# Optimization experiments

Measured on AMD Instinct MI355X. Metric: run time of the kernel, lower is better.

## Reference

```python
import jax, jax.numpy as jnp
import numpy as np

STRIDE, PAD, DIL = 1, 1, 1


def setup_inputs() -> dict:
    key = jax.random.key(0)
    ks = jax.random.split(key, 5)
    N, Cin, H, W = 8, 256, 56, 56
    Cout, kh, kw = 256, 3, 3
    x = jax.random.normal(ks[0], (N, Cin, H, W), jnp.float32)
    offset = jax.random.normal(ks[1], (N, 2 * kh * kw, H, W), jnp.float32)
    mask = jax.random.uniform(ks[2], (N, kh * kw, H, W), jnp.float32)
    fan_in = Cin * kh * kw
    bound = float(np.sqrt(6.0 / fan_in))  # kaiming_uniform, relu gain
    weight = jax.random.uniform(ks[3], (Cout, Cin, kh, kw), jnp.float32, -bound, bound)
    bias = jnp.zeros((Cout,), jnp.float32)
    return {"x": x, "offset": offset, "mask": mask, "weight": weight, "bias": bias}


def _mdcn(x, offset, mask, weight, bias):
    N, Cin, H, W = x.shape
    Cout, _, kh, kw = weight.shape
    K = kh * kw
    Hout = (H + 2 * PAD - (DIL * (kh - 1) + 1)) // STRIDE + 1
    Wout = (W + 2 * PAD - (DIL * (kw - 1) + 1)) // STRIDE + 1
    # offset channels: [K, 2(y,x)] interleaved -> [N,K,2,Hout,Wout]
    off = offset.reshape(N, K, 2, Hout, Wout)
    dy, dx = off[:, :, 0], off[:, :, 1]
    ky = (jnp.arange(K) // kw) * DIL
    kx = (jnp.arange(K) % kw) * DIL
    base_y = jnp.arange(Hout) * STRIDE - PAD
    base_x = jnp.arange(Wout) * STRIDE - PAD
    py = dy + ky[None, :, None, None] + base_y[None, None, :, None]  # [N,K,Ho,Wo]
    px = dx + kx[None, :, None, None] + base_x[None, None, None, :]
    y0 = jnp.floor(py)
    x0 = jnp.floor(px)
    wy1 = py - y0
    wx1 = px - x0
    wy0 = 1.0 - wy1
    wx0 = 1.0 - wx1
    y0i = y0.astype(jnp.int32)
    x0i = x0.astype(jnp.int32)
    x_nhwc = jnp.transpose(x, (0, 2, 3, 1))  # [N,H,W,Cin]
    nidx = jnp.arange(N)[:, None, None, None]

    def gather(yi, xi):
        valid = (yi >= 0) & (yi < H) & (xi >= 0) & (xi < W)
        yc = jnp.clip(yi, 0, H - 1)
        xc = jnp.clip(xi, 0, W - 1)
        v = x_nhwc[nidx, yc, xc]  # [N,K,Ho,Wo,Cin]
        return v * valid[..., None].astype(x.dtype)

    v = (gather(y0i, x0i) * (wy0 * wx0)[..., None]
         + gather(y0i, x0i + 1) * (wy0 * wx1)[..., None]
         + gather(y0i + 1, x0i) * (wy1 * wx0)[..., None]
         + gather(y0i + 1, x0i + 1) * (wy1 * wx1)[..., None])
    v = v * mask.reshape(N, K, Hout, Wout)[..., None]
    wr = weight.reshape(Cout, Cin, K)
    out = jnp.einsum('nkhwc,ock->nohw', v, wr)
    return out + bias[None, :, None, None]


def reference(x, offset, mask, weight, bias):
    return _mdcn(x, offset, mask, weight, bias)
```

## Files before the change

kernel.cpp:

```cpp
#include <hip/hip_runtime.h>
#include <math.h>

#define H_ 56
#define W_ 56
#define CIN 256
#define COUT 256
#define NB 8
#define SPIX 3136
#define KG 2304
#define MTOT 25088
#define MT 128
#define NBLK 196
#define GUARD_PX 2048

typedef __bf16 v8bf __attribute__((ext_vector_type(8)));
typedef float  v4f  __attribute__((ext_vector_type(4)));

#define WAIT_VM(N)  do { asm volatile("s_waitcnt vmcnt(" #N ")" ::: "memory"); \
                         __builtin_amdgcn_sched_barrier(0); } while (0)
#define WAIT_LGKM0  do { asm volatile("s_waitcnt lgkmcnt(0)" ::: "memory"); \
                         __builtin_amdgcn_sched_barrier(0); } while (0)
#define BARR        do { asm volatile("s_barrier" ::: "memory"); } while (0)

__device__ __forceinline__ void async_copy16(const void* g, void* l) {
    __builtin_amdgcn_global_load_lds(
        (const __attribute__((address_space(1))) void*)g,
        (__attribute__((address_space(3))) void*)l, 16, 0, 0);
}

__global__ __launch_bounds__(256) void prep_xw(const float* __restrict__ x,
                                               const float* __restrict__ w,
                                               __bf16* __restrict__ xb,
                                               __bf16* __restrict__ bp) {
    __shared__ float tile[64][65];
    const int tid = threadIdx.x;
    if (blockIdx.z < 8) {
        const int n = blockIdx.z, c0 = blockIdx.y * 64, s0 = blockIdx.x * 64;
        const float* xp = x + (size_t)n * CIN * SPIX;
        __bf16* xo = xb + (size_t)n * SPIX * CIN;
#pragma unroll
        for (int i = 0; i < 16; ++i) {
            int idx = tid + i * 256;
            int cr = idx >> 6, sc = idx & 63;
            tile[cr][sc] = xp[(c0 + cr) * SPIX + s0 + sc];
        }
        __syncthreads();
#pragma unroll
        for (int i = 0; i < 16; ++i) {
            int idx = tid + i * 256;
            int sr = idx >> 6, cc = idx & 63;
            xo[(s0 + sr) * CIN + c0 + cc] = (__bf16)tile[cc][sr];
        }
    } else {
        const int base = (blockIdx.y * 49 + blockIdx.x) * 256 + tid;
        for (int i = base; i < COUT * KG; i += 196 * 256) {
            const int o = i / KG;
            const int rem = i - o * KG;
            const int c = rem / 9;
            const int tap = rem - c * 9;
            bp[(size_t)o * KG + tap * 256 + c] = (__bf16)w[i];
        }
    }
}

__device__ __forceinline__ void compute_params(
    const float* __restrict__ offs, const float* __restrict__ msk,
    int m0, int* sS, float4* sW, int tid)
{
    for (int idx = tid; idx < 9 * MT; idx += 512) {
        const int tl = idx >> 7, pl = idx & 127;
        const int pg = m0 + pl;
        const int n  = pg / SPIX;
        const int s  = pg - n * SPIX;
        const int h  = s / W_, w = s - h * W_;
        const int kY = tl / 3, kX = tl - kY * 3;
        const float dy = offs[n * (18 * SPIX) + (2 * tl) * SPIX + s];
        const float dx = offs[n * (18 * SPIX) + (2 * tl + 1) * SPIX + s];
        const float mk = msk[n * (9 * SPIX) + tl * SPIX + s];
        const float py = dy + (float)(kY + h - 1);
        const float px = dx + (float)(kX + w - 1);
        const float fy0 = floorf(py), fx0 = floorf(px);
        const int y0 = (int)fy0, x0 = (int)fx0;
        const float wy1 = py - fy0, wx1 = px - fx0;
        const float wy0 = 1.f - wy1, wx0 = 1.f - wx1;
        const bool yv0 = (y0 >= 0) & (y0 < H_);
        const bool yv1 = (y0 + 1 >= 0) & (y0 + 1 < H_);
        const bool xv0 = (x0 >= 0) & (x0 < W_);
        const bool xv1 = (x0 + 1 >= 0) & (x0 + 1 < W_);
        float4 wt;
        wt.x = (yv0 & xv0) ? wy0 * wx0 * mk : 0.f;
        wt.y = (yv0 & xv1) ? wy0 * wx1 * mk : 0.f;
        wt.z = (yv1 & xv0) ? wy1 * wx0 * mk : 0.f;
        wt.w = (yv1 & xv1) ? wy1 * wx1 * mk : 0.f;
        int base = n * SPIX + y0 * W_ + x0;
        base = min(max(base, -GUARD_PX), NB * SPIX - 58 + GUARD_PX);
        sS[idx] = base * CIN;
        sW[idx] = wt;
    }
}

__global__ __launch_bounds__(512, 2) void mdcn_fused4(
    const __bf16* __restrict__ xb,
    const float*  __restrict__ offs,
    const float*  __restrict__ msk,
    const __bf16* __restrict__ bp,
    const float*  __restrict__ bias,
    float*        __restrict__ out)
{
    __shared__ __align__(16) char smem[121344];
    int*    sS = (int*)(smem + 98304);
    float4* sW = (float4*)(smem + 102912);

    const int tid  = threadIdx.x;
    const int lane = tid & 63, wv = tid >> 6;
    const int wm = wv & 1, wn = wv >> 1;
    const int l15 = lane & 15, q = lane >> 4;

    const int xcd = blockIdx.x & 7, ib = blockIdx.x >> 3;
    const int wg  = (xcd < 4) ? xcd * 25 + ib : 100 + (xcd - 4) * 24 + ib;
    const int m0  = wg * MT;

    compute_params(offs, msk, m0, sS, sW, tid);

    v4f acc[4][4];
#pragma unroll
    for (int i = 0; i < 4; ++i)
#pragma unroll
        for (int j = 0; j < 4; ++j) acc[i][j] = (v4f)0.f;

    __syncthreads();

    const int pxl = tid >> 2, c2 = tid & 3;
    v8bf ga0, ga1, ga2, ga3, gb0, gb1, gb2, gb3;
    float4 cw;

#define GATHER(E, KQ)                                                   \
    { const int b_ = sS[E] + ((KQ) << 6) + c2 * 8;                      \
      cw  = sW[E];                                                      \
      ga0 = *(const v8bf*)(xb + b_);                                    \
      ga1 = *(const v8bf*)(xb + b_ + 256);                              \
      ga2 = *(const v8bf*)(xb + b_ + 14336);                            \
      ga3 = *(const v8bf*)(xb + b_ + 14592);                            \
      gb0 = *(const v8bf*)(xb + b_ + 32);                               \
      gb1 = *(const v8bf*)(xb + b_ + 288);                              \
      gb2 = *(const v8bf*)(xb + b_ + 14368);                            \
      gb3 = *(const v8bf*)(xb + b_ + 14624); }

#define COMBINE_STORE(AP)                                               \
    { v8bf r0, r1;                                                      \
      _Pragma("unroll")                                                 \
      for (int j = 0; j < 8; ++j) {                                     \
        r0[j] = (__bf16)(cw.x * (float)ga0[j] + cw.y * (float)ga1[j]    \
                       + cw.z * (float)ga2[j] + cw.w * (float)ga3[j]);  \
        r1[j] = (__bf16)(cw.x * (float)gb0[j] + cw.y * (float)gb1[j]    \
                       + cw.z * (float)gb2[j] + cw.w * (float)gb3[j]);  \
      }                                                                 \
      *(v8bf*)((AP) + pxl * 64 + (((c2)     ^ (pxl & 7)) << 3)) = r0;   \
      *(v8bf*)((AP) + pxl * 64 + (((c2 + 4) ^ (pxl & 7)) << 3)) = r1; }

#define STAGE_B(K0, LB)                                                 \
    { _Pragma("unroll")                                                 \
      for (int t = 0; t < 4; ++t) {                                     \
        const int brow = t * 64 + (wv << 3) + (lane >> 3);              \
        const int blc  = (lane & 7) ^ (brow & 7);                       \
        async_copy16(bp + (size_t)brow * KG + (K0) + blc * 8,           \
                     (LB) + ((t * 8 + wv) << 10)); }

    GATHER(pxl, 0)
    COMBINE_STORE((__bf16*)smem)
    STAGE_B(0, smem + 32768) }
    GATHER(pxl, 1)
    WAIT_LGKM0;
    WAIT_VM(8);
    BARR;

    char* ac = smem;          char* an = smem + 16384;
    char* bc = smem + 32768;  char* bn = smem + 65536;

#pragma unroll 1
    for (int ks = 0; ks < 36; ++ks) {
        if (ks < 35) {
            STAGE_B((ks + 1) << 6, bn) }
            WAIT_VM(4);
            COMBINE_STORE((__bf16*)an)
            if (ks < 34) {
                const int st = ks + 2;
                GATHER((st >> 2) * MT + pxl, st & 3)
            }
        }

        __builtin_amdgcn_s_setprio(1);
#pragma unroll
        for (int kf = 0; kf < 2; ++kf) {
            v8bf afr[4], bfr[4];
#pragma unroll
            for (int mt = 0; mt < 4; ++mt) {
                const int row = wm * 64 + mt * 16 + l15;
                const int pch = (kf * 4 + q) ^ (row & 7);
                afr[mt] = *(const v8bf*)((__bf16*)ac + row * 64 + pch * 8);
            }
#pragma unroll
            for (int nt = 0; nt < 4; ++nt) {
                const int row = wn * 64 + nt * 16 + l15;
                const int pch = (kf * 4 + q) ^ (row & 7);
                bfr[nt] = *(const v8bf*)((__bf16*)bc + row * 64 + pch * 8);
            }
#pragma unroll
            for (int mt = 0; mt < 4; ++mt)
#pragma unroll
                for (int nt = 0; nt < 4; ++nt)
                    acc[mt][nt] = __builtin_amdgcn_mfma_f32_16x16x32_bf16(
                        afr[mt], bfr[nt], acc[mt][nt], 0, 0, 0);
        }
        __builtin_amdgcn_s_setprio(0);

        if (ks < 34) {
            WAIT_LGKM0;
            WAIT_VM(8);
            BARR;
        } else if (ks == 34) {
            WAIT_LGKM0;
            WAIT_VM(0);
            BARR;
        }
        char* t;
        t = ac; ac = an; an = t;
        t = bc; bc = bn; bn = t;
    }
#undef GATHER
#undef COMBINE_STORE
#undef STAGE_B

    WAIT_LGKM0;
    BARR;
    float* epi = (float*)smem + wv * 1104;
    const int pg_l = m0 + wm * 64 + lane;
    const int n_l  = pg_l / SPIX;
    float* outp = out + (size_t)n_l * (COUT * SPIX) + (pg_l - n_l * SPIX);

#pragma unroll
    for (int nt = 0; nt < 4; ++nt) {
        const float bv = bias[wn * 64 + nt * 16 + l15];
#pragma unroll
        for (int mt = 0; mt < 4; ++mt)
#pragma unroll
            for (int r = 0; r < 4; ++r)
                epi[(mt * 16 + q * 4 + r) * 17 + l15] = acc[mt][nt][r] + bv;
#pragma unroll
        for (int oc = 0; oc < 16; ++oc)
            outp[(size_t)(wn * 64 + nt * 16 + oc) * SPIX] = epi[lane * 17 + oc];
    }
}

#define BM 64
#define BN 64
#define BKF 32
#define AST 68
#define BST 68
#define CST 65
__global__ __launch_bounds__(256) void mdcn_fallback(
    const float* __restrict__ xs, const float* __restrict__ offs,
    const float* __restrict__ msk, const float* __restrict__ wraw,
    const float* __restrict__ bias, float* __restrict__ out)
{
    __shared__ float smem[BKF * AST + BKF * BST];
    __shared__ int   sBase[4][BM];
    __shared__ float sWgt[4][BM];
    float (*At)[AST] = (float (*)[AST])smem;
    float (*Bt)[BST] = (float (*)[BST])(smem + BKF * AST);
    float (*Cs)[CST] = (float (*)[CST])smem;
    const int tid = threadIdx.x;
    const int m0 = blockIdx.x * BM;
    const int o0 = blockIdx.y * BN;
    const int n  = m0 / SPIX;
    const int s0 = m0 - n * SPIX;
    const int tx = tid & 15, ty = tid >> 4;
    float acc[4][4] = {};
    for (int k = 0; k < 9; ++k) {
        if (tid < BM) {
            const int s = s0 + tid;
            const int h = s / W_;
            const int w = s - h * W_;
            const int kY = k / 3, kX = k - kY * 3;
            const float dy = offs[(size_t)n * (18 * SPIX) + (size_t)(2 * k) * SPIX + s];
            const float dx = offs[(size_t)n * (18 * SPIX) + (size_t)(2 * k + 1) * SPIX + s];
            const float mk = msk[(size_t)n * (9 * SPIX) + (size_t)k * SPIX + s];
            const float py = dy + (float)(kY + h - 1);
            const float px = dx + (float)(kX + w - 1);
            const float fy0 = floorf(py), fx0 = floorf(px);
            const int y0 = (int)fy0, x0 = (int)fx0;
            const float wy1 = py - fy0, wx1 = px - fx0;
            const float wy0 = 1.0f - wy1, wx0 = 1.0f - wx1;
#pragma unroll
            for (int t = 0; t < 4; ++t) {
                const int yi = y0 + (t >> 1), xi = x0 + (t & 1);
                const bool valid = (yi >= 0) & (yi < H_) & (xi >= 0) & (xi < W_);
                const int yc = min(max(yi, 0), H_ - 1);
                const int xc = min(max(xi, 0), W_ - 1);
                float wt = ((t >> 1) ? wy1 : wy0) * ((t & 1) ? wx1 : wx0) * mk;
                sBase[t][tid] = n * (CIN * SPIX) + yc * W_ + xc;
                sWgt[t][tid] = valid ? wt : 0.0f;
            }
        }
        __syncthreads();
        for (int c0 = 0; c0 < CIN; c0 += BKF) {
#pragma unroll
            for (int i = 0; i < 8; ++i) {
                int idx = tid + i * 256;
                int row = idx >> 5, cc = idx & 31;
                int ce = (c0 + cc) * SPIX;
                At[cc][row] = sWgt[0][row] * xs[sBase[0][row] + ce]
                            + sWgt[1][row] * xs[sBase[1][row] + ce]
                            + sWgt[2][row] * xs[sBase[2][row] + ce]
                            + sWgt[3][row] * xs[sBase[3][row] + ce];
            }
#pragma unroll
            for (int i = 0; i < 8; ++i) {
                int idx = tid + i * 256;
                int kf = idx >> 6, o = idx & 63;
                Bt[kf][o] = wraw[(size_t)(o0 + o) * KG + (c0 + kf) * 9 + k];
            }
            __syncthreads();
#pragma unroll
            for (int kf = 0; kf < BKF; ++kf) {
                const float4 a = *(const float4*)&At[kf][ty * 4];
                const float4 b = *(const float4*)&Bt[kf][tx * 4];
                acc[0][0] = fmaf(a.x, b.x, acc[0][0]); acc[0][1] = fmaf(a.x, b.y, acc[0][1]);
                acc[0][2] = fmaf(a.x, b.z, acc[0][2]); acc[0][3] = fmaf(a.x, b.w, acc[0][3]);
                acc[1][0] = fmaf(a.y, b.x, acc[1][0]); acc[1][1] = fmaf(a.y, b.y, acc[1][1]);
                acc[1][2] = fmaf(a.y, b.z, acc[1][2]); acc[1][3] = fmaf(a.y, b.w, acc[1][3]);
                acc[2][0] = fmaf(a.z, b.x, acc[2][0]); acc[2][1] = fmaf(a.z, b.y, acc[2][1]);
                acc[2][2] = fmaf(a.z, b.z, acc[2][2]); acc[2][3] = fmaf(a.z, b.w, acc[2][3]);
                acc[3][0] = fmaf(a.w, b.x, acc[3][0]); acc[3][1] = fmaf(a.w, b.y, acc[3][1]);
                acc[3][2] = fmaf(a.w, b.z, acc[3][2]); acc[3][3] = fmaf(a.w, b.w, acc[3][3]);
            }
            __syncthreads();
        }
    }
#pragma unroll
    for (int i = 0; i < 4; ++i)
#pragma unroll
        for (int j = 0; j < 4; ++j)
            Cs[ty * 4 + i][tx * 4 + j] = acc[i][j] + bias[o0 + tx * 4 + j];
    __syncthreads();
    const int pix = tid & 63, ob = tid >> 6;
    float* outp = out + (size_t)n * COUT * SPIX + s0 + pix;
#pragma unroll
    for (int r = 0; r < 16; ++r) {
        int o = r * 4 + ob;
        outp[(size_t)(o0 + o) * SPIX] = Cs[pix][o];
    }
}

extern "C" void kernel_launch(void* const* d_in, const int* in_sizes, int n_in,
                              void* d_out, int out_size, void* d_ws, size_t ws_size,
                              hipStream_t stream) {
    const float* x    = (const float*)d_in[0];
    const float* offs = (const float*)d_in[1];
    const float* msk  = (const float*)d_in[2];
    const float* w    = (const float*)d_in[3];
    const float* bias = (const float*)d_in[4];
    float* out = (float*)d_out;

    const size_t GUARD_B  = (size_t)GUARD_PX * CIN * sizeof(__bf16);
    const size_t xb_bytes = (size_t)NB * SPIX * CIN * sizeof(__bf16);
    const size_t bp_bytes = (size_t)KG * COUT * sizeof(__bf16);
    const size_t need     = GUARD_B + xb_bytes + GUARD_B + bp_bytes;

    if (ws_size >= need) {
        __bf16* xb = (__bf16*)((char*)d_ws + GUARD_B);
        __bf16* bp = (__bf16*)((char*)d_ws + GUARD_B + xb_bytes + GUARD_B);
        hipMemsetAsync(d_ws, 0, GUARD_B, stream);
        hipMemsetAsync((char*)d_ws + GUARD_B + xb_bytes, 0, GUARD_B, stream);
        prep_xw<<<dim3(49, 4, 9), 256, 0, stream>>>(x, w, xb, bp);
        mdcn_fused4<<<dim3(NBLK), 512, 0, stream>>>(xb, offs, msk, bp, bias, out);
    } else {
        mdcn_fallback<<<dim3(MTOT / BM, COUT / BN), 256, 0, stream>>>(
            x, offs, msk, w, bias, out);
    }
}
```

Measured before the change: 156.0 us.

## Triple-buffer weight tiles, double-register gather, fold guard memsets into prep kernel

```diff
diff --git a/kernel.cpp b/kernel.cpp
--- a/kernel.cpp
+++ b/kernel.cpp
@@ -51,7 +51,7 @@
             int sr = idx >> 6, cc = idx & 63;
             xo[(s0 + sr) * CIN + c0 + cc] = (__bf16)tile[cc][sr];
         }
-    } else {
+    } else if (blockIdx.z == 8) {
         const int base = (blockIdx.y * 49 + blockIdx.x) * 256 + tid;
         for (int i = base; i < COUT * KG; i += 196 * 256) {
             const int o = i / KG;
@@ -59,6 +59,15 @@
             const int c = rem / 9;
             const int tap = rem - c * 9;
             bp[(size_t)o * KG + tap * 256 + c] = (__bf16)w[i];
+        }
+    } else {
+        const int gtid = (blockIdx.y * 49 + blockIdx.x) * 256 + tid;
+        v8bf* lo = (v8bf*)(xb - (size_t)GUARD_PX * CIN);
+        v8bf* hi = (v8bf*)(xb + (size_t)NB * SPIX * CIN);
+        const v8bf z = (v8bf)(__bf16)0.f;
+        for (int i = gtid; i < 65536; i += 196 * 256) {
+            lo[i] = z;
+            hi[i] = z;
         }
     }
 }
@@ -99,7 +108,7 @@
     }
 }
 
-__global__ __launch_bounds__(512, 2) void mdcn_fused4(
+__global__ __launch_bounds__(512, 2) void mdcn_fused5(
     const __bf16* __restrict__ xb,
     const float*  __restrict__ offs,
     const float*  __restrict__ msk,
@@ -107,9 +116,11 @@
     const float*  __restrict__ bias,
     float*        __restrict__ out)
 {
-    __shared__ __align__(16) char smem[121344];
-    int*    sS = (int*)(smem + 98304);
-    float4* sW = (float4*)(smem + 102912);
+    __shared__ __align__(16) char smem[154112];
+    __bf16* A0 = (__bf16*)smem;
+    __bf16* A1 = (__bf16*)(smem + 16384);
+    int*    sS = (int*)(smem + 131072);
+    float4* sW = (float4*)(smem + 135680);
 
     const int tid  = threadIdx.x;
     const int lane = tid & 63, wv = tid >> 6;
@@ -130,106 +141,119 @@
 
     __syncthreads();
 
-    const int pxl = tid >> 2, c2 = tid & 3;
-    v8bf ga0, ga1, ga2, ga3, gb0, gb1, gb2, gb3;
-    float4 cw;
-
-#define GATHER(E, KQ)                                                   \
-    { const int b_ = sS[E] + ((KQ) << 6) + c2 * 8;                      \
-      cw  = sW[E];                                                      \
-      ga0 = *(const v8bf*)(xb + b_);                                    \
-      ga1 = *(const v8bf*)(xb + b_ + 256);                              \
-      ga2 = *(const v8bf*)(xb + b_ + 14336);                            \
-      ga3 = *(const v8bf*)(xb + b_ + 14592);                            \
-      gb0 = *(const v8bf*)(xb + b_ + 32);                               \
-      gb1 = *(const v8bf*)(xb + b_ + 288);                              \
-      gb2 = *(const v8bf*)(xb + b_ + 14368);                            \
-      gb3 = *(const v8bf*)(xb + b_ + 14624); }
-
-#define COMBINE_STORE(AP)                                               \
-    { v8bf r0, r1;                                                      \
-      _Pragma("unroll")                                                 \
-      for (int j = 0; j < 8; ++j) {                                     \
-        r0[j] = (__bf16)(cw.x * (float)ga0[j] + cw.y * (float)ga1[j]    \
-                       + cw.z * (float)ga2[j] + cw.w * (float)ga3[j]);  \
-        r1[j] = (__bf16)(cw.x * (float)gb0[j] + cw.y * (float)gb1[j]    \
-                       + cw.z * (float)gb2[j] + cw.w * (float)gb3[j]);  \
-      }                                                                 \
-      *(v8bf*)((AP) + pxl * 64 + (((c2)     ^ (pxl & 7)) << 3)) = r0;   \
-      *(v8bf*)((AP) + pxl * 64 + (((c2 + 4) ^ (pxl & 7)) << 3)) = r1; }
-
-#define STAGE_B(K0, LB)                                                 \
-    { _Pragma("unroll")                                                 \
-      for (int t = 0; t < 4; ++t) {                                     \
-        const int brow = t * 64 + (wv << 3) + (lane >> 3);              \
-        const int blc  = (lane & 7) ^ (brow & 7);                       \
-        async_copy16(bp + (size_t)brow * KG + (K0) + blc * 8,           \
-                     (LB) + ((t * 8 + wv) << 10)); }
-
-    GATHER(pxl, 0)
-    COMBINE_STORE((__bf16*)smem)
-    STAGE_B(0, smem + 32768) }
-    GATHER(pxl, 1)
+    const int pq = tid >> 3, c8 = tid & 7;
+    const int offA0 = pq * 64 + ((c8 ^ (pq & 7)) << 3);
+    const int offA1 = offA0 + 4096;
+    v8bf ga0A, ga1A, ga2A, ga3A, gb0A, gb1A, gb2A, gb3A;
+    v8bf ga0B, ga1B, ga2B, ga3B, gb0B, gb1B, gb2B, gb3B;
+
+#define GATHER2(S, J)                                                    \
+    { const int e0_ = ((J) >> 2) * 128 + pq;                             \
+      const int ko_ = (((J) & 3) << 6) + (c8 << 3);                      \
+      const int b0_ = sS[e0_] + ko_;                                     \
+      const int b1_ = sS[e0_ + 64] + ko_;                                \
+      ga0##S = *(const v8bf*)(xb + b0_);                                 \
+      ga1##S = *(const v8bf*)(xb + b0_ + 256);                           \
+      ga2##S = *(const v8bf*)(xb + b0_ + 14336);                         \
+      ga3##S = *(const v8bf*)(xb + b0_ + 14592);                         \
+      gb0##S = *(const v8bf*)(xb + b1_);                                 \
+      gb1##S = *(const v8bf*)(xb + b1_ + 256);                           \
+      gb2##S = *(const v8bf*)(xb + b1_ + 14336);                         \
+      gb3##S = *(const v8bf*)(xb + b1_ + 14592); }
+
+#define COMBINE2(S, J, AP)                                               \
+    { const int e0_ = ((J) >> 2) * 128 + pq;                             \
+      const float4 wa_ = sW[e0_];                                        \
+      const float4 wb_ = sW[e0_ + 64];                                   \
+      v8bf r0_, r1_;                                                     \
+      _Pragma("unroll")                                                  \
+      for (int j = 0; j < 8; ++j) {                                      \
+        r0_[j] = (__bf16)(wa_.x * (float)ga0##S[j] + wa_.y * (float)ga1##S[j] \
+                        + wa_.z * (float)ga2##S[j] + wa_.w * (float)ga3##S[j]); \
+        r1_[j] = (__bf16)(wb_.x * (float)gb0##S[j] + wb_.y * (float)gb1##S[j] \
+                        + wb_.z * (float)gb2##S[j] + wb_.w * (float)gb3##S[j]); } \
+      *(v8bf*)((AP) + offA0) = r0_;                                      \
+      *(v8bf*)((AP) + offA1) = r1_; }
+
+#define STAGE_B(K0, LB)                                                  \
+    do { _Pragma("unroll")                                               \
+      for (int t = 0; t < 4; ++t) {                                      \
+        const int brow = t * 64 + (wv << 3) + (lane >> 3);               \
+        const int blc  = (lane & 7) ^ (brow & 7);                        \
+        async_copy16(bp + (size_t)brow * KG + (K0) + blc * 8,            \
+                     (LB) + ((t * 8 + wv) << 10)); } } while (0)
+
+#define MFMA_STEP(AB, BB)                                                \
+    { __builtin_amdgcn_s_setprio(1);                                     \
+      _Pragma("unroll")                                                  \
+      for (int kf = 0; kf < 2; ++kf) {                                   \
+        v8bf afr[4], bfr[4];                                             \
+        _Pragma("unroll")                                                \
+        for (int mt = 0; mt < 4; ++mt) {                                 \
+          const int row = wm * 64 + mt * 16 + l15;                       \
+          const int pch = (kf * 4 + q) ^ (row & 7);                      \
+          afr[mt] = *(const v8bf*)((AB) + row * 64 + pch * 8); }         \
+        _Pragma("unroll")                                                \
+        for (int nt = 0; nt < 4; ++nt) {                                 \
+          const int row = wn * 64 + nt * 16 + l15;                       \
+          const int pch = (kf * 4 + q) ^ (row & 7);                      \
+          bfr[nt] = *(const v8bf*)((BB) + row * 64 + pch * 8); }         \
+        _Pragma("unroll")                                                \
+        for (int mt = 0; mt < 4; ++mt)                                   \
+          _Pragma("unroll")                                              \
+          for (int nt = 0; nt < 4; ++nt)                                 \
+            acc[mt][nt] = __builtin_amdgcn_mfma_f32_16x16x32_bf16(       \
+                afr[mt], bfr[nt], acc[mt][nt], 0, 0, 0); }               \
+      __builtin_amdgcn_s_setprio(0); }
+
+    STAGE_B(0, smem + 32768);
+    GATHER2(A, 0)
+    STAGE_B(64, smem + 65536);
+    WAIT_VM(4);
+    COMBINE2(A, 0, A0)
+    GATHER2(B, 1)
     WAIT_LGKM0;
-    WAIT_VM(8);
     BARR;
 
-    char* ac = smem;          char* an = smem + 16384;
-    char* bc = smem + 32768;  char* bn = smem + 65536;
+    __bf16* bc = (__bf16*)(smem + 32768);
+    __bf16* bn = (__bf16*)(smem + 65536);
+    __bf16* b2 = (__bf16*)(smem + 98304);
 
 #pragma unroll 1
-    for (int ks = 0; ks < 36; ++ks) {
-        if (ks < 35) {
-            STAGE_B((ks + 1) << 6, bn) }
-            WAIT_VM(4);
-            COMBINE_STORE((__bf16*)an)
-            if (ks < 34) {
-                const int st = ks + 2;
-                GATHER((st >> 2) * MT + pxl, st & 3)
-            }
-        }
-
-        __builtin_amdgcn_s_setprio(1);
-#pragma unroll
-        for (int kf = 0; kf < 2; ++kf) {
-            v8bf afr[4], bfr[4];
-#pragma unroll
-            for (int mt = 0; mt < 4; ++mt) {
-                const int row = wm * 64 + mt * 16 + l15;
-                const int pch = (kf * 4 + q) ^ (row & 7);
-                afr[mt] = *(const v8bf*)((__bf16*)ac + row * 64 + pch * 8);
-            }
-#pragma unroll
-            for (int nt = 0; nt < 4; ++nt) {
-                const int row = wn * 64 + nt * 16 + l15;
-                const int pch = (kf * 4 + q) ^ (row & 7);
-                bfr[nt] = *(const v8bf*)((__bf16*)bc + row * 64 + pch * 8);
-            }
-#pragma unroll
-            for (int mt = 0; mt < 4; ++mt)
-#pragma unroll
-                for (int nt = 0; nt < 4; ++nt)
-                    acc[mt][nt] = __builtin_amdgcn_mfma_f32_16x16x32_bf16(
-                        afr[mt], bfr[nt], acc[mt][nt], 0, 0, 0);
-        }
-        __builtin_amdgcn_s_setprio(0);
-
-        if (ks < 34) {
-            WAIT_LGKM0;
-            WAIT_VM(8);
-            BARR;
-        } else if (ks == 34) {
-            WAIT_LGKM0;
-            WAIT_VM(0);
-            BARR;
-        }
-        char* t;
-        t = ac; ac = an; an = t;
-        t = bc; bc = bn; bn = t;
-    }
-#undef GATHER
-#undef COMBINE_STORE
+    for (int k2 = 0; k2 < 17; ++k2) {
+        const int e = k2 * 2;
+        STAGE_B((size_t)(e + 2) << 6, (char*)b2);
+        GATHER2(A, e + 2)
+        WAIT_VM(12);
+        COMBINE2(B, e + 1, A1)
+        MFMA_STEP(A0, bc);
+        WAIT_LGKM0;
+        BARR;
+        { __bf16* t = bc; bc = bn; bn = b2; b2 = t; }
+
+        const int o = e + 1;
+        STAGE_B((size_t)(o + 2) << 6, (char*)b2);
+        GATHER2(B, o + 2)
+        WAIT_VM(12);
+        COMBINE2(A, o + 1, A0)
+        MFMA_STEP(A1, bc);
+        WAIT_LGKM0;
+        BARR;
+        { __bf16* t = bc; bc = bn; bn = b2; b2 = t; }
+    }
+
+    WAIT_VM(0);
+    COMBINE2(B, 35, A1)
+    MFMA_STEP(A0, bc);
+    WAIT_LGKM0;
+    BARR;
+    { __bf16* t = bc; bc = bn; bn = b2; b2 = t; }
+    MFMA_STEP(A1, bc);
+
+#undef GATHER2
+#undef COMBINE2
 #undef STAGE_B
+#undef MFMA_STEP
 
     WAIT_LGKM0;
     BARR;
@@ -370,10 +394,8 @@
     if (ws_size >= need) {
         __bf16* xb = (__bf16*)((char*)d_ws + GUARD_B);
         __bf16* bp = (__bf16*)((char*)d_ws + GUARD_B + xb_bytes + GUARD_B);
-        hipMemsetAsync(d_ws, 0, GUARD_B, stream);
-        hipMemsetAsync((char*)d_ws + GUARD_B + xb_bytes, 0, GUARD_B, stream);
-        prep_xw<<<dim3(49, 4, 9), 256, 0, stream>>>(x, w, xb, bp);
-        mdcn_fused4<<<dim3(NBLK), 512, 0, stream>>>(xb, offs, msk, bp, bias, out);
+        prep_xw<<<dim3(49, 4, 10), 256, 0, stream>>>(x, w, xb, bp);
+        mdcn_fused5<<<dim3(NBLK), 512, 0, stream>>>(xb, offs, msk, bp, bias, out);
     } else {
         mdcn_fallback<<<dim3(MTOT / BM, COUT / BN), 256, 0, stream>>>(
             x, offs, msk, w, bias, out);
```

Result: slower. 159.4 us (+2.2%).
